# Performance work log

Hardware: AMD Instinct MI355X
Metric: run time of the kernel (lower is better)

The kernel has to match this reference:

```python
import jax, jax.numpy as jnp
import numpy as np

B, CIN, COUT, H, W = 4, 256, 256, 96, 96
GN_GROUPS = 16
EPS = 1e-5


def setup_inputs() -> dict:
    key = jax.random.key(0)
    k0, k1, k2, k3 = jax.random.split(key, 4)
    x = jax.random.normal(k0, (B, CIN, H, W), jnp.float32)
    offset = jax.random.normal(k1, (B, 18, H, W), jnp.float32)
    mask = jax.random.uniform(k2, (B, 9, H, W), jnp.float32)  # modulation scalars (sigmoid-range)
    weight = jax.random.normal(k3, (COUT, CIN, 3, 3), jnp.float32) * 0.02
    gamma = jnp.ones((COUT,), jnp.float32)
    beta = jnp.zeros((COUT,), jnp.float32)
    return {"x": x, "offset": offset, "mask": mask, "weight": weight, "gamma": gamma, "beta": beta}


def _bilinear(xf, py, px, Hs, Ws):
    # xf: [B, C, H*W] flattened input; py/px: [B, H, W] sample coords -> [B, C, H, W]
    y0 = jnp.floor(py)
    x0 = jnp.floor(px)
    acc = jnp.zeros((xf.shape[0], xf.shape[1], py.shape[1], py.shape[2]), xf.dtype)
    for dy in (0, 1):
        for dx in (0, 1):
            yy = y0 + dy
            xx = x0 + dx
            wgt = (1.0 - jnp.abs(py - yy)) * (1.0 - jnp.abs(px - xx))
            valid = (yy >= 0) & (yy < Hs) & (xx >= 0) & (xx < Ws)  # zero-pad outside
            yi = jnp.clip(yy, 0, Hs - 1).astype(jnp.int32)
            xi = jnp.clip(xx, 0, Ws - 1).astype(jnp.int32)
            idx = (yi * Ws + xi).reshape(py.shape[0], -1)  # [B, H*W]
            g = jax.vmap(lambda xb, ib: xb[:, ib])(xf, idx)  # [B, C, H*W]
            g = g.reshape(acc.shape)
            acc = acc + g * (wgt * valid.astype(xf.dtype))[:, None]
    return acc


def _modulated_deform_conv(x, offset, mask, weight):
    # 3x3, stride=1, pad=1, dilation=1, deform_groups=1, no bias
    Bz, C, Hs, Ws = x.shape
    hh = jnp.arange(Hs, dtype=x.dtype)
    ww = jnp.arange(Ws, dtype=x.dtype)
    base_y, base_x = jnp.meshgrid(hh, ww, indexing="ij")  # [H, W]
    xf = x.reshape(Bz, C, Hs * Ws)
    out = jnp.zeros((Bz, weight.shape[0], Hs, Ws), x.dtype)
    for k in range(9):  # fixed 3x3 kernel taps
        ki, kj = k // 3, k % 3
        py = base_y[None] + (ki - 1) + offset[:, 2 * k]      # dy channel
        px = base_x[None] + (kj - 1) + offset[:, 2 * k + 1]  # dx channel
        val = _bilinear(xf, py, px, Hs, Ws) * mask[:, k][:, None]  # [B, CIN, H, W]
        out = out + jnp.einsum("oc,bchw->bohw", weight[:, :, ki, kj], val)
    return out


def _group_norm(x, gamma, beta):
    Bz, C, Hs, Ws = x.shape
    xr = x.reshape(Bz, GN_GROUPS, C // GN_GROUPS, Hs, Ws)
    mu = xr.mean(axis=(2, 3, 4), keepdims=True)
    var = xr.var(axis=(2, 3, 4), keepdims=True)
    xn = ((xr - mu) * jax.lax.rsqrt(var + EPS)).reshape(Bz, C, Hs, Ws)
    return xn * gamma[None, :, None, None] + beta[None, :, None, None]


def reference(x, offset, mask, weight, gamma, beta):
    y = _modulated_deform_conv(x, offset, mask, weight)
    return _group_norm(y, gamma, beta)
```

## Files before the change

kernel.cpp:

```cpp
#include <hip/hip_runtime.h>
#include <hip/hip_bf16.h>
#include <cstdint>

typedef short    short8  __attribute__((ext_vector_type(8)));
typedef ushort   ushort8 __attribute__((ext_vector_type(8)));
typedef float    f32x4   __attribute__((ext_vector_type(4)));
typedef _Float16 half8   __attribute__((ext_vector_type(8)));

#define BATCH 4
#define CIN   256
#define COUT  256
#define HH    96
#define WW    96
#define HWSZ  9216
#define GN_G  16
#define EPSV  1e-5f
#define BN    144
#define NPB   64
#define NWG   (BATCH*NPB)

__device__ __forceinline__ float bf2f(ushort u) {
    return __uint_as_float(((uint32_t)u) << 16);
}
__device__ __forceinline__ ushort f2bf(float f) {
    uint32_t u = __float_as_uint(f);
    u += 0x7FFFu + ((u >> 16) & 1u);
    return (ushort)(u >> 16);
}

__global__ __launch_bounds__(256)
void nhwc_kernel(const float* __restrict__ x, _Float16* __restrict__ xn) {
    __shared__ _Float16 tile[64][66];
    const int b  = blockIdx.z;
    const int cb = blockIdx.y * 64;
    const int pb = blockIdx.x * 64;
    const int t  = threadIdx.x;
    {
        const int pl = t & 63;
        const int cq = t >> 6;
        #pragma unroll
        for (int i = 0; i < 16; ++i) {
            const int c = cq * 16 + i;
            tile[c][pl] = (_Float16)x[((size_t)b * CIN + cb + c) * HWSZ + pb + pl];
        }
    }
    __syncthreads();
    {
        const int cl = t & 63;
        const int pq = t >> 6;
        #pragma unroll
        for (int i = 0; i < 16; ++i) {
            const int p = pq * 16 + i;
            xn[((size_t)b * HWSZ + pb + p) * CIN + cb + cl] = tile[cl][p];
        }
    }
}

__global__ __launch_bounds__(256)
void repack_w_kernel(const float* __restrict__ w, ushort* __restrict__ wp) {
    const int d    = blockIdx.x * 256 + threadIdx.x;
    const int j    = d & 7;
    const int cout = (d >> 3) & 255;
    const int kb8  = d >> 11;
    const int ktap = kb8 >> 5;
    const int cin  = ((kb8 & 31) << 3) | j;
    wp[d] = f2bf(w[cout * (CIN * 9) + cin * 9 + ktap]);
}

__global__ __launch_bounds__(512, 2)
void dcn_mfma_kernel(const _Float16* __restrict__ xn, const float* __restrict__ off,
                     const float* __restrict__ msk, const ushort* __restrict__ wp,
                     float* __restrict__ out, ushort* __restrict__ yb, int use_bf16,
                     float* __restrict__ part) {
    __shared__ __align__(16) ushort buf[2][BN * 128];
    __shared__ int    s_idx[2][BN][4];
    __shared__ float  s_wgt[2][BN][4];

    const int bid  = blockIdx.x;
    const int swz  = (bid & 7) * (NWG / 8) + (bid >> 3);
    const int b    = swz / NPB;
    const int pblk = swz - b * NPB;
    const int p0   = pblk * BN;

    const int t    = threadIdx.x;
    const int lane = t & 63;
    const int wid  = t >> 6;
    const int cgp  = wid & 3;
    const int kh   = wid >> 2;

    auto coords = [&](int k) {
        if (t < BN) {
            const int slot = k & 1;
            const int pos  = p0 + t;
            const int hh   = pos / WW;
            const int ww   = pos - hh * WW;
            const size_t obase = ((size_t)b * 18 + 2 * k) * HWSZ + pos;
            const float oy = off[obase];
            const float ox = off[obase + HWSZ];
            const float m  = msk[((size_t)b * 9 + k) * HWSZ + pos];
            const float py = (float)(hh + k / 3 - 1) + oy;
            const float px = (float)(ww + k % 3 - 1) + ox;
            const float y0 = floorf(py), x0 = floorf(px);
            #pragma unroll
            for (int dy = 0; dy < 2; ++dy)
                #pragma unroll
                for (int dx = 0; dx < 2; ++dx) {
                    const float yy = y0 + (float)dy, xx = x0 + (float)dx;
                    const float wb = (1.f - fabsf(py - yy)) * (1.f - fabsf(px - xx));
                    const bool valid = (yy >= 0.f) && (yy < (float)HH) && (xx >= 0.f) && (xx < (float)WW);
                    int yi = (int)yy; yi = yi < 0 ? 0 : (yi > HH - 1 ? HH - 1 : yi);
                    int xi = (int)xx; xi = xi < 0 ? 0 : (xi > WW - 1 ? WW - 1 : xi);
                    s_idx[slot][t][dy * 2 + dx] = yi * WW + xi;
                    s_wgt[slot][t][dy * 2 + dx] = valid ? wb * m : 0.f;
                }
        }
    };

    const int sp  = lane >> 4;
    const int c16 = lane & 15;
    auto stage = [&](int c, ushort* dstbuf) {
        const int tap  = c >> 1;
        const int half = c & 1;
        const int slot = tap & 1;
        const _Float16* xb = xn + (size_t)b * HWSZ * CIN + half * 128 + c16 * 8;
        #pragma unroll
        for (int g = 0; g < 5; ++g) {
            const bool active = (g < 4) || (sp < 2);
            const int p = wid * 18 + ((g < 4) ? (g * 4 + sp) : (16 + sp));
            if (active) {
                const _Float16 w0 = (_Float16)s_wgt[slot][p][0];
                const _Float16 w1 = (_Float16)s_wgt[slot][p][1];
                const _Float16 w2 = (_Float16)s_wgt[slot][p][2];
                const _Float16 w3 = (_Float16)s_wgt[slot][p][3];
                const half8 v0 = *(const half8*)(xb + (size_t)s_idx[slot][p][0] * CIN);
                const half8 v1 = *(const half8*)(xb + (size_t)s_idx[slot][p][1] * CIN);
                const half8 v2 = *(const half8*)(xb + (size_t)s_idx[slot][p][2] * CIN);
                const half8 v3 = *(const half8*)(xb + (size_t)s_idx[slot][p][3] * CIN);
                const half8 h = v0 * w0 + v1 * w1 + v2 * w2 + v3 * w3;
                ushort8 o;
                #pragma unroll
                for (int j = 0; j < 8; j += 2) {
                    const __hip_bfloat162 h2 =
                        __float22bfloat162_rn(float2{(float)h[j], (float)h[j + 1]});
                    const uint32_t u = *reinterpret_cast<const uint32_t*>(&h2);
                    o[j]     = (ushort)u;
                    o[j + 1] = (ushort)(u >> 16);
                }
                char* drow = (char*)dstbuf + p * 256;
                *(ushort8*)(drow + ((c16 * 16) ^ ((p & 15) << 4))) = o;
            }
        }
    };

    f32x4 acc[4][9];
    #pragma unroll
    for (int i = 0; i < 4; ++i)
        #pragma unroll
        for (int j = 0; j < 9; ++j)
            acc[i][j] = (f32x4){0.f, 0.f, 0.f, 0.f};

    const int arow = lane & 15;
    const int akb  = lane >> 4;

    auto loadA = [&](int kb8base, int ks, short8 af[4]) {
        const ushort* wrow = wp + ((size_t)(kb8base + ks * 4 + akb) * COUT + cgp * 64 + arow) * 8;
        #pragma unroll
        for (int mt = 0; mt < 4; ++mt)
            af[mt] = *(const short8*)(wrow + mt * 16 * 8);
    };

    auto mfma_chunk = [&](int kb8base, const ushort* src, short8 afA[4]) {
        const char* srow = (const char*)src;
        short8 afB[4];
        #pragma unroll
        for (int ks = 0; ks < 2; ++ks) {
            const int ksg = kh * 2 + ks;
            if (ks == 0) loadA(kb8base, kh * 2 + 1, afB);
            short8* afc = ks ? afB : afA;
            #pragma unroll
            for (int nt = 0; nt < 9; ++nt) {
                const int row = arow + nt * 16;
                const short8 bfr = *(const short8*)(srow + row * 256 + ((ksg * 64 + akb * 16) ^ ((row & 15) << 4)));
                #pragma unroll
                for (int mt = 0; mt < 4; ++mt)
                    acc[mt][nt] = __builtin_amdgcn_mfma_f32_16x16x32_bf16(
                        afc[mt], bfr, acc[mt][nt], 0, 0, 0);
            }
        }
    };

    coords(0);
    __syncthreads();
    stage(0, buf[0]);
    __syncthreads();
    for (int c = 0; c < 18; ++c) {
        if (c < 17) stage(c + 1, buf[(c + 1) & 1]);
        if (!(c & 1) && (c >> 1) + 1 < 9) coords((c >> 1) + 1);
        short8 afA[4];
        loadA(c * 16, kh * 2, afA);
        mfma_chunk(c * 16, buf[c & 1], afA);
        __syncthreads();
    }

    {
        f32x4* s_xch = reinterpret_cast<f32x4*>(&buf[0][0]);
        const int plane = cgp * 64 + lane;
        #pragma unroll
        for (int mt = 0; mt < 4; ++mt) {
            if (wid >= 4) {
                #pragma unroll
                for (int nt = 0; nt < 9; ++nt)
                    s_xch[plane * 10 + nt] = acc[mt][nt];
            }
            __syncthreads();
            if (wid < 4) {
                #pragma unroll
                for (int nt = 0; nt < 9; ++nt)
                    acc[mt][nt] += s_xch[plane * 10 + nt];
            }
            __syncthreads();
        }
    }

    if (wid < 4) {
        const int prow = lane & 15;
        const int crow = (lane >> 4) * 4;
        if (use_bf16) {
            #pragma unroll
            for (int mt = 0; mt < 4; ++mt) {
                const int cout = cgp * 64 + mt * 16 + crow;
                #pragma unroll
                for (int nt = 0; nt < 9; ++nt) {
                    const int opos = p0 + nt * 16 + prow;
                    ushort* op = yb + ((size_t)b * COUT + cout) * HWSZ + opos;
                    #pragma unroll
                    for (int r = 0; r < 4; ++r)
                        op[(size_t)r * HWSZ] = f2bf(acc[mt][nt][r]);
                }
            }
        } else {
            #pragma unroll
            for (int mt = 0; mt < 4; ++mt) {
                const int cout = cgp * 64 + mt * 16 + crow;
                #pragma unroll
                for (int nt = 0; nt < 9; ++nt) {
                    const int opos = p0 + nt * 16 + prow;
                    float* op = out + ((size_t)b * COUT + cout) * HWSZ + opos;
                    #pragma unroll
                    for (int r = 0; r < 4; ++r)
                        op[(size_t)r * HWSZ] = acc[mt][nt][r];
                }
            }
        }

        #pragma unroll
        for (int mt = 0; mt < 4; ++mt) {
            float s = 0.f, q = 0.f;
            #pragma unroll
            for (int nt = 0; nt < 9; ++nt)
                #pragma unroll
                for (int r = 0; r < 4; ++r) {
                    const float v = acc[mt][nt][r];
                    s += v; q += v * v;
                }
            #pragma unroll
            for (int o = 32; o > 0; o >>= 1) {
                s += __shfl_xor(s, o);
                q += __shfl_xor(q, o);
            }
            if (lane == 0) {
                const int bg = b * GN_G + cgp * 4 + mt;
                part[((size_t)bg * NPB + pblk) * 2]     = s;
                part[((size_t)bg * NPB + pblk) * 2 + 1] = q;
            }
        }
    }
}

__global__ __launch_bounds__(256)
void gn_apply_bf16_kernel(const ushort* __restrict__ yb, const float* __restrict__ part,
                          const float* __restrict__ gamma, const float* __restrict__ beta,
                          float* __restrict__ out) {
    __shared__ float sm[2];
    const int bg = blockIdx.y;
    const int t  = threadIdx.x;
    if (t < 64) {
        float s = part[((size_t)bg * NPB + t) * 2];
        float q = part[((size_t)bg * NPB + t) * 2 + 1];
        #pragma unroll
        for (int o = 32; o > 0; o >>= 1) {
            s += __shfl_xor(s, o);
            q += __shfl_xor(q, o);
        }
        if (t == 0) {
            const float invn = 1.f / (float)((COUT / GN_G) * HWSZ);
            const float mean = s * invn;
            const float var  = q * invn - mean * mean;
            sm[0] = mean;
            sm[1] = rsqrtf(var + EPSV);
        }
    }
    __syncthreads();
    const float mean = sm[0], inv = sm[1];
    const size_t base = (size_t)bg * (COUT / GN_G) * HWSZ + (size_t)blockIdx.x * 16384;
    #pragma unroll 2
    for (int it = 0; it < 8; ++it) {
        const size_t e = base + ((size_t)(it * 256 + t)) * 8;
        const int c = (int)((e / HWSZ) & (COUT - 1));
        const float sc = inv * gamma[c];
        const float sh = beta[c] - mean * sc;
        const ushort8 v = *(const ushort8*)(yb + e);
        float4 o0, o1;
        o0.x = bf2f(v[0]) * sc + sh;  o0.y = bf2f(v[1]) * sc + sh;
        o0.z = bf2f(v[2]) * sc + sh;  o0.w = bf2f(v[3]) * sc + sh;
        o1.x = bf2f(v[4]) * sc + sh;  o1.y = bf2f(v[5]) * sc + sh;
        o1.z = bf2f(v[6]) * sc + sh;  o1.w = bf2f(v[7]) * sc + sh;
        *(float4*)(out + e)     = o0;
        *(float4*)(out + e + 4) = o1;
    }
}

__global__ __launch_bounds__(256)
void gn_apply_f32_kernel(float* __restrict__ y, const float* __restrict__ part,
                         const float* __restrict__ gamma, const float* __restrict__ beta) {
    __shared__ float sm[2];
    const int bg = blockIdx.y;
    const int t  = threadIdx.x;
    if (t < 64) {
        float s = part[((size_t)bg * NPB + t) * 2];
        float q = part[((size_t)bg * NPB + t) * 2 + 1];
        #pragma unroll
        for (int o = 32; o > 0; o >>= 1) {
            s += __shfl_xor(s, o);
            q += __shfl_xor(q, o);
        }
        if (t == 0) {
            const float invn = 1.f / (float)((COUT / GN_G) * HWSZ);
            const float mean = s * invn;
            const float var  = q * invn - mean * mean;
            sm[0] = mean;
            sm[1] = rsqrtf(var + EPSV);
        }
    }
    __syncthreads();
    const float mean = sm[0], inv = sm[1];
    const size_t base = (size_t)bg * (COUT / GN_G) * HWSZ + (size_t)blockIdx.x * 16384;
    #pragma unroll 2
    for (int it = 0; it < 16; ++it) {
        const size_t e = base + ((size_t)(it * 256 + t)) * 4;
        const int c = (int)((e / HWSZ) & (COUT - 1));
        const float sc = inv * gamma[c];
        const float sh = beta[c] - mean * sc;
        float4 v = *(float4*)(y + e);
        v.x = v.x * sc + sh;  v.y = v.y * sc + sh;
        v.z = v.z * sc + sh;  v.w = v.w * sc + sh;
        *(float4*)(y + e) = v;
    }
}

extern "C" void kernel_launch(void* const* d_in, const int* in_sizes, int n_in,
                              void* d_out, int out_size, void* d_ws, size_t ws_size,
                              hipStream_t stream) {
    const float* x      = (const float*)d_in[0];
    const float* offset = (const float*)d_in[1];
    const float* mask   = (const float*)d_in[2];
    const float* weight = (const float*)d_in[3];
    const float* gamma  = (const float*)d_in[4];
    const float* beta   = (const float*)d_in[5];
    float* out = (float*)d_out;

    const size_t XN = (size_t)BATCH * HWSZ * CIN;
    const size_t WP = (size_t)9 * CIN * COUT;
    const size_t PT = (size_t)BATCH * GN_G * NPB * 2;
    _Float16* xn   = (_Float16*)d_ws;
    ushort*   wp   = (ushort*)d_ws + XN;
    float*    part = (float*)((ushort*)d_ws + XN + WP);
    ushort*   yb   = (ushort*)(part + PT);
    const size_t need = (XN + WP) * 2 + PT * 4 + (size_t)BATCH * COUT * HWSZ * 2;
    const int use_bf16 = (ws_size >= need) ? 1 : 0;

    {
        dim3 g(HWSZ / 64, CIN / 64, BATCH);
        nhwc_kernel<<<g, 256, 0, stream>>>(x, xn);
    }
    repack_w_kernel<<<9 * CIN * COUT / 256, 256, 0, stream>>>(weight, wp);

    dcn_mfma_kernel<<<NWG, 512, 0, stream>>>(xn, offset, mask, wp, out, yb, use_bf16, part);

    dim3 gg(9, BATCH * GN_G);
    if (use_bf16)
        gn_apply_bf16_kernel<<<gg, 256, 0, stream>>>(yb, part, gamma, beta, out);
    else
        gn_apply_f32_kernel<<<gg, 256, 0, stream>>>(out, part, gamma, beta);
}
```

Baseline: 95.50 us.

## Stage full 256-channel tap per pipeline step, halving barrier count

The main loop now processes one full kernel tap (all 256 input channels) per iteration instead of half a tap, so it runs 9 iterations with 9 barriers rather than 18. Each stage call gathers both channel halves using the same four bilinear indices and weights, and coordinates are now computed two taps ahead. The trade-off is that the LDS staging buffer doubles in size, which may lower occupancy below the 2 blocks per CU requested by the launch bounds, and more work sits between each pair of barriers.

```diff
diff --git a/kernel.cpp b/kernel.cpp
--- a/kernel.cpp
+++ b/kernel.cpp
@@ -72,7 +72,7 @@
                      const float* __restrict__ msk, const ushort* __restrict__ wp,
                      float* __restrict__ out, ushort* __restrict__ yb, int use_bf16,
                      float* __restrict__ part) {
-    __shared__ __align__(16) ushort buf[2][BN * 128];
+    __shared__ __align__(16) ushort buf[2][BN * 256];
     __shared__ int    s_idx[2][BN][4];
     __shared__ float  s_wgt[2][BN][4];
 
@@ -118,36 +118,41 @@
 
     const int sp  = lane >> 4;
     const int c16 = lane & 15;
-    auto stage = [&](int c, ushort* dstbuf) {
-        const int tap  = c >> 1;
-        const int half = c & 1;
-        const int slot = tap & 1;
-        const _Float16* xb = xn + (size_t)b * HWSZ * CIN + half * 128 + c16 * 8;
+    auto stage = [&](int k, ushort* dstbuf) {
+        const int slot = k & 1;
+        const _Float16* xb0 = xn + (size_t)b * HWSZ * CIN + c16 * 8;
         #pragma unroll
         for (int g = 0; g < 5; ++g) {
             const bool active = (g < 4) || (sp < 2);
             const int p = wid * 18 + ((g < 4) ? (g * 4 + sp) : (16 + sp));
             if (active) {
+                const int i0 = s_idx[slot][p][0], i1 = s_idx[slot][p][1];
+                const int i2 = s_idx[slot][p][2], i3 = s_idx[slot][p][3];
                 const _Float16 w0 = (_Float16)s_wgt[slot][p][0];
                 const _Float16 w1 = (_Float16)s_wgt[slot][p][1];
                 const _Float16 w2 = (_Float16)s_wgt[slot][p][2];
                 const _Float16 w3 = (_Float16)s_wgt[slot][p][3];
-                const half8 v0 = *(const half8*)(xb + (size_t)s_idx[slot][p][0] * CIN);
-                const half8 v1 = *(const half8*)(xb + (size_t)s_idx[slot][p][1] * CIN);
-                const half8 v2 = *(const half8*)(xb + (size_t)s_idx[slot][p][2] * CIN);
-                const half8 v3 = *(const half8*)(xb + (size_t)s_idx[slot][p][3] * CIN);
-                const half8 h = v0 * w0 + v1 * w1 + v2 * w2 + v3 * w3;
-                ushort8 o;
-                #pragma unroll
-                for (int j = 0; j < 8; j += 2) {
-                    const __hip_bfloat162 h2 =
-                        __float22bfloat162_rn(float2{(float)h[j], (float)h[j + 1]});
-                    const uint32_t u = *reinterpret_cast<const uint32_t*>(&h2);
-                    o[j]     = (ushort)u;
-                    o[j + 1] = (ushort)(u >> 16);
+                char* drow = (char*)dstbuf + p * 512;
+                const int sw = (p & 15) << 4;
+                #pragma unroll
+                for (int half = 0; half < 2; ++half) {
+                    const _Float16* xb = xb0 + half * 128;
+                    const half8 v0 = *(const half8*)(xb + (size_t)i0 * CIN);
+                    const half8 v1 = *(const half8*)(xb + (size_t)i1 * CIN);
+                    const half8 v2 = *(const half8*)(xb + (size_t)i2 * CIN);
+                    const half8 v3 = *(const half8*)(xb + (size_t)i3 * CIN);
+                    const half8 h = v0 * w0 + v1 * w1 + v2 * w2 + v3 * w3;
+                    ushort8 o;
+                    #pragma unroll
+                    for (int j = 0; j < 8; j += 2) {
+                        const __hip_bfloat162 h2 =
+                            __float22bfloat162_rn(float2{(float)h[j], (float)h[j + 1]});
+                        const uint32_t u = *reinterpret_cast<const uint32_t*>(&h2);
+                        o[j]     = (ushort)u;
+                        o[j + 1] = (ushort)(u >> 16);
+                    }
+                    *(ushort8*)(drow + ((c16 * 16 + half * 256) ^ sw)) = o;
                 }
-                char* drow = (char*)dstbuf + p * 256;
-                *(ushort8*)(drow + ((c16 * 16) ^ ((p & 15) << 4))) = o;
             }
         }
     };
@@ -162,25 +167,26 @@
     const int arow = lane & 15;
     const int akb  = lane >> 4;
 
-    auto loadA = [&](int kb8base, int ks, short8 af[4]) {
-        const ushort* wrow = wp + ((size_t)(kb8base + ks * 4 + akb) * COUT + cgp * 64 + arow) * 8;
+    auto loadA = [&](int kb8base, int ksg, short8 af[4]) {
+        const ushort* wrow = wp + ((size_t)(kb8base + ksg * 4 + akb) * COUT + cgp * 64 + arow) * 8;
         #pragma unroll
         for (int mt = 0; mt < 4; ++mt)
             af[mt] = *(const short8*)(wrow + mt * 16 * 8);
     };
 
-    auto mfma_chunk = [&](int kb8base, const ushort* src, short8 afA[4]) {
+    auto mfma_tap = [&](int kb8base, const ushort* src, short8 afA[4]) {
         const char* srow = (const char*)src;
         short8 afB[4];
         #pragma unroll
-        for (int ks = 0; ks < 2; ++ks) {
-            const int ksg = kh * 2 + ks;
-            if (ks == 0) loadA(kb8base, kh * 2 + 1, afB);
-            short8* afc = ks ? afB : afA;
+        for (int ks = 0; ks < 4; ++ks) {
+            const int ksg = kh * 4 + ks;
+            if (ks < 3) loadA(kb8base, kh * 4 + ks + 1, (ks & 1) ? afA : afB);
+            short8* afc = (ks & 1) ? afB : afA;
+            const int bfull = ksg * 64 + akb * 16;
             #pragma unroll
             for (int nt = 0; nt < 9; ++nt) {
                 const int row = arow + nt * 16;
-                const short8 bfr = *(const short8*)(srow + row * 256 + ((ksg * 64 + akb * 16) ^ ((row & 15) << 4)));
+                const short8 bfr = *(const short8*)(srow + row * 512 + (bfull ^ ((row & 15) << 4)));
                 #pragma unroll
                 for (int mt = 0; mt < 4; ++mt)
                     acc[mt][nt] = __builtin_amdgcn_mfma_f32_16x16x32_bf16(
@@ -192,13 +198,14 @@
     coords(0);
     __syncthreads();
     stage(0, buf[0]);
+    coords(1);
     __syncthreads();
-    for (int c = 0; c < 18; ++c) {
-        if (c < 17) stage(c + 1, buf[(c + 1) & 1]);
-        if (!(c & 1) && (c >> 1) + 1 < 9) coords((c >> 1) + 1);
+    for (int k = 0; k < 9; ++k) {
+        if (k < 8) stage(k + 1, buf[(k + 1) & 1]);
+        if (k + 2 <= 8) coords(k + 2);
         short8 afA[4];
-        loadA(c * 16, kh * 2, afA);
-        mfma_chunk(c * 16, buf[c & 1], afA);
+        loadA(k * 32, kh * 4, afA);
+        mfma_tap(k * 32, buf[k & 1], afA);
         __syncthreads();
     }
 
```

Result: no change. 95.66 us (+0.2%).
